# Optimization experiments

Hardware: AMD Instinct MI355X
Metric: run time of the kernel (lower is better)

Reference implementation:

```python
import jax, jax.numpy as jnp
import numpy as np
from jax import lax

B_SZ, SEQ, D_MODEL, D_STATE, DT_RANK = 4, 4096, 256, 16, 16


def setup_inputs() -> dict:
    key = jax.random.key(0)
    ks = jax.random.split(key, 12)
    d, n, r = D_MODEL, D_STATE, DT_RANK
    inp = {}
    inp["hidden_states"] = jax.random.normal(ks[0], (B_SZ, SEQ, d), jnp.float32)
    inp["in_proj_w"] = jax.random.normal(ks[1], (3 * d, d), jnp.float32) * (d ** -0.5)
    inp["x_proj_w"] = jax.random.normal(ks[2], (r + 2 * n, d), jnp.float32) * (d ** -0.5)
    s = r ** -0.5
    inp["dt_proj_w"] = jax.random.uniform(ks[3], (d, r), jnp.float32, -s, s)
    dt = jnp.exp(jax.random.uniform(ks[4], (d,), jnp.float32) * (np.log(0.1) - np.log(1e-3)) + np.log(1e-3))
    inp["dt_proj_b"] = dt + jnp.log(-jnp.expm1(-dt))  # inverse-softplus init
    inp["A_log"] = jnp.log(jnp.broadcast_to(jnp.arange(1, n + 1, dtype=jnp.float32), (d, n)))
    inp["D"] = jnp.ones((d,), jnp.float32)
    inp["out_proj1_w"] = jax.random.normal(ks[5], (d, d), jnp.float32) * (d ** -0.5)
    inp["conv_x_w"] = jax.random.normal(ks[6], (d, 1, 1), jnp.float32)
    inp["conv_x_b"] = jax.random.normal(ks[7], (d,), jnp.float32) * 0.1
    inp["conv_y_w"] = jax.random.normal(ks[8], (d, 1, 3), jnp.float32) * (3 ** -0.5)
    inp["conv_y_b"] = jax.random.normal(ks[9], (d,), jnp.float32) * 0.1
    inp["conv_z_w"] = jax.random.normal(ks[10], (d, 1, 5), jnp.float32) * (5 ** -0.5)
    inp["conv_z_b"] = jax.random.normal(ks[11], (d,), jnp.float32) * 0.1
    return inp


def _silu(x):
    return x * jax.nn.sigmoid(x)


def _dwconv(x, w, b):
    # x: (b, d, l); w: (d, 1, k) depthwise; 'same' padding (odd k)
    k = w.shape[-1]
    pad = (k - 1) // 2
    out = lax.conv_general_dilated(
        x, w, window_strides=(1,), padding=[(pad, pad)],
        dimension_numbers=("NCH", "OIH", "NCH"), feature_group_count=x.shape[1])
    return out + b[None, :, None]


def _selective_scan(u, delta, A, B, C, D, delta_bias):
    # u, delta: (b,d,l); A: (d,n); B,C: (b,n,l); D, delta_bias: (d,)
    delta = jax.nn.softplus(delta + delta_bias[None, :, None])
    dA = jnp.exp(jnp.einsum("bdl,dn->lbdn", delta, A))          # (l,b,d,n)
    dBu = jnp.einsum("bdl,bnl,bdl->lbdn", delta, B, u)           # (l,b,d,n)
    Ct = jnp.transpose(C, (2, 0, 1))                             # (l,b,n)

    def step(h, inp):
        dA_t, dBu_t, C_t = inp
        h = dA_t * h + dBu_t                                     # (b,d,n)
        y = jnp.einsum("bdn,bn->bd", h, C_t)
        return h, y

    h0 = jnp.zeros(u.shape[:2] + (A.shape[1],), u.dtype)
    _, ys = lax.scan(step, h0, (dA, dBu, Ct))                    # ys: (l,b,d)
    y = jnp.transpose(ys, (1, 2, 0))                             # (b,d,l)
    return y + D[None, :, None] * u


def reference(hidden_states, in_proj_w, x_proj_w, dt_proj_w, dt_proj_b, A_log, D,
              out_proj1_w, conv_x_w, conv_x_b, conv_y_w, conv_y_b, conv_z_w, conv_z_b):
    b, l, d = hidden_states.shape
    xyz = jnp.einsum("ble,de->bdl", hidden_states, in_proj_w)    # (b, 3d, l)
    x, y, z = jnp.split(xyz, 3, axis=1)                          # each (b,d,l)
    A = -jnp.exp(A_log.astype(jnp.float32))
    x = _silu(_dwconv(x, conv_x_w, conv_x_b))
    y = _silu(_dwconv(y, conv_y_w, conv_y_b))
    z = _silu(_dwconv(z, conv_z_w, conv_z_b))
    x_dbl = jnp.einsum("bdl,ed->ble", x, x_proj_w)               # (b,l,r+2n)
    dt_r, Bm, Cm = jnp.split(x_dbl, [DT_RANK, DT_RANK + D_STATE], axis=-1)
    # dt_proj applies bias here; selective_scan adds delta_bias again (faithful to source)
    dt = jnp.einsum("blr,dr->bdl", dt_r, dt_proj_w) + dt_proj_b[None, :, None]
    Bm = jnp.transpose(Bm, (0, 2, 1))                            # (b,n,l)
    Cm = jnp.transpose(Cm, (0, 2, 1))
    p = _selective_scan(x, dt, A, Bm, Cm, D.astype(jnp.float32), dt_proj_b.astype(jnp.float32))
    p = jnp.transpose(p, (0, 2, 1))                              # (b,l,d)
    y = jnp.transpose(y, (0, 2, 1))
    z = jnp.transpose(z, (0, 2, 1))
    l1 = jnp.einsum("bld,ed->ble", p * y, out_proj1_w)
    l2 = l1 * z
    l2 = _dwconv(jnp.transpose(l2, (0, 2, 1)), conv_x_w, conv_x_b)
    return jnp.transpose(l2, (0, 2, 1))                          # (b,l,d)
```

## Files before the change

kernel.cpp:

```cpp
#include <hip/hip_runtime.h>
#include <hip/hip_bf16.h>
#include <math.h>

typedef __hip_bfloat16 bf16;
typedef __attribute__((ext_vector_type(8))) short bf16x8;
typedef __attribute__((ext_vector_type(4))) float f32x4;

#define B_SZ 4
#define SEQ  4096
#define DM   256
#define NST  16
#define NCHK 64
#define LC   (SEQ/NCHK)
#define MT   (B_SZ*SEQ)
#define CT   4
#define NLIN (B_SZ*16*256)

__device__ __forceinline__ float silu_f(float v){ return v / (1.f + __expf(-v)); }
__device__ __forceinline__ float softplus_f(float v){
  return (v > 15.f) ? v : __logf(1.f + __expf(v));
}
__device__ __forceinline__ short f2bf(float f){
  union { bf16 h; short s; } u; u.h = __float2bfloat16(f); return u.s;
}
__device__ __forceinline__ float bf2f(short s){
  union { unsigned int i; float f; } v;
  v.i = ((unsigned int)(unsigned short)s) << 16; return v.f;
}
__device__ __forceinline__ float4 bf4_to_f4(uint2 q){
  float4 f;
  f.x = bf2f((short)(q.x & 0xffffu)); f.y = bf2f((short)(q.x >> 16));
  f.z = bf2f((short)(q.y & 0xffffu)); f.w = bf2f((short)(q.y >> 16));
  return f;
}
__device__ __forceinline__ short4 f4_to_bf4(float4 f){
  short4 s; s.x = f2bf(f.x); s.y = f2bf(f.y); s.z = f2bf(f.z); s.w = f2bf(f.w);
  return s;
}

__device__ __forceinline__ void async_cp16(const short* g, short* l){
  __builtin_amdgcn_global_load_lds(
      (const __attribute__((address_space(1))) unsigned int*)g,
      (__attribute__((address_space(3))) unsigned int*)l, 16, 0, 0);
}

template<int CTRL>
__device__ __forceinline__ float dpp_add_step(float v){
  int x = __builtin_amdgcn_update_dpp(0, __float_as_int(v), CTRL, 0xf, 0xf, true);
  return v + __int_as_float(x);
}

__global__ __launch_bounds__(256)
void cvt_in_k(const float* __restrict__ w_in, const float* __restrict__ w_o1,
              const float* __restrict__ hs,
              short* __restrict__ w_in_b, short* __restrict__ w_o1_b,
              short* __restrict__ hsb)
{
  int i = blockIdx.x * 256 + threadIdx.x;
  if (i < 49152) {
    float4 q = *(const float4*)&w_in[i * 4];
    *(short4*)&w_in_b[i * 4] = f4_to_bf4(q);
  } else if (i < 65536) {
    int j = i - 49152;
    float4 q = *(const float4*)&w_o1[j * 4];
    *(short4*)&w_o1_b[j * 4] = f4_to_bf4(q);
  } else {
    int j = i - 65536;
    float4 q = *(const float4*)&hs[(size_t)j * 4];
    *(short4*)&hsb[(size_t)j * 4] = f4_to_bf4(q);
  }
}

template<int EPI, bool OBF>
__global__ __launch_bounds__(256)
void mfma_gemm_k(const short* __restrict__ Av, const short* __restrict__ Bw,
                 void* __restrict__ Outv, int N, int K,
                 const float* __restrict__ bias, const short* __restrict__ zc,
                 const float* __restrict__ cwx)
{
  constexpr int BM = 128, BN = 128, BK = 64;
  __shared__ short As[BM * BK];
  __shared__ short Bs[BN * BK];
  const int tid  = threadIdx.x;
  const int wave = tid >> 6, lane = tid & 63;
  const int quad = lane >> 4, l16 = lane & 15;
  const int wm = (wave & 1) * 64, wn = (wave >> 1) * 64;
  const int m0 = blockIdx.x * BM, n0 = blockIdx.y * BN;

  f32x4 acc[4][4] = {};

  for (int k0 = 0; k0 < K; k0 += BK) {
    #pragma unroll
    for (int p = 0; p < 4; p++) {
      int id = p * 256 + tid;
      int row = id >> 3, slot = id & 7;
      int gch = slot ^ (row & 7);
      async_cp16(Av + (size_t)(m0 + row) * K + k0 + gch * 8,
                 &As[row * 64 + slot * 8]);
      async_cp16(Bw + (size_t)(n0 + row) * K + k0 + gch * 8,
                 &Bs[row * 64 + slot * 8]);
    }
    __syncthreads();
    #pragma unroll
    for (int ks = 0; ks < 2; ks++) {
      bf16x8 fa[4], fb[4];
      #pragma unroll
      for (int i = 0; i < 4; i++) {
        int sa = (ks * 4 + quad) ^ (l16 & 7);
        fa[i] = *(const bf16x8*)&As[(wm + i * 16 + l16) * 64 + sa * 8];
        fb[i] = *(const bf16x8*)&Bs[(wn + i * 16 + l16) * 64 + sa * 8];
      }
      #pragma unroll
      for (int i = 0; i < 4; i++)
        #pragma unroll
        for (int j = 0; j < 4; j++)
          acc[i][j] = __builtin_amdgcn_mfma_f32_16x16x32_bf16(fa[i], fb[j], acc[i][j], 0, 0, 0);
    }
    __syncthreads();
  }

  #pragma unroll
  for (int i = 0; i < 4; i++) {
    #pragma unroll
    for (int j = 0; j < 4; j++) {
      int n = n0 + wn + j * 16 + l16;
      #pragma unroll
      for (int r = 0; r < 4; r++) {
        int m = m0 + wm + i * 16 + quad * 4 + r;
        float v = acc[i][j][r];
        if constexpr (EPI == 2)
          v = v * bf2f(zc[(size_t)m * N + n]) * cwx[n] + bias[n];
        if constexpr (OBF) ((short*)Outv)[(size_t)m * N + n] = f2bf(v);
        else               ((float*)Outv)[(size_t)m * N + n] = v;
      }
    }
  }
}

__global__ __launch_bounds__(256)
void gemm34_k(const short* __restrict__ xcb,
              const float* __restrict__ Bw,
              const float* __restrict__ wdt,
              const float* __restrict__ bdt,
              float* __restrict__ xdbl,
              float* __restrict__ dtv)
{
  constexpr int TM = 32, TK = 16, NN = 48;
  __shared__ __align__(16) float As[TK][TM + 4];
  __shared__ __align__(16) float Bs[TK][64 + 4];
  __shared__ __align__(16) float dt_s[TM][20];
  __shared__ __align__(16) float wdt_s[256][20];
  const int tid = threadIdx.x;
  const int tn = tid & 15, tm = tid >> 4;
  const int m0 = blockIdx.x * TM;
  float acc[2][4] = {};
  const int mlA = tid >> 3, kdA = (tid & 7) * 2;
  const int mlB = tid >> 2, kqB = (tid & 3) * 4;

  {
    float4 q0 = *(const float4*)&wdt[tid * 16 + 0];
    float4 q1 = *(const float4*)&wdt[tid * 16 + 4];
    float4 q2 = *(const float4*)&wdt[tid * 16 + 8];
    float4 q3 = *(const float4*)&wdt[tid * 16 + 12];
    *(float4*)&wdt_s[tid][0]  = q0;
    *(float4*)&wdt_s[tid][4]  = q1;
    *(float4*)&wdt_s[tid][8]  = q2;
    *(float4*)&wdt_s[tid][12] = q3;
  }

  for (int k0 = 0; k0 < 256; k0 += TK) {
    {
      size_t off = (size_t)(m0 + mlA) * 256 + k0 + kdA;
      unsigned int v = *(const unsigned int*)(xcb + off);
      As[kdA + 0][mlA] = bf2f((short)(v & 0xffffu));
      As[kdA + 1][mlA] = bf2f((short)(v >> 16));
    }
    {
      float v0 = 0.f, v1 = 0.f, v2 = 0.f, v3 = 0.f;
      if (mlB < NN) {
        float4 q = *(const float4*)(Bw + (size_t)mlB * 256 + k0 + kqB);
        v0 = q.x; v1 = q.y; v2 = q.z; v3 = q.w;
      }
      Bs[kqB+0][mlB] = v0; Bs[kqB+1][mlB] = v1; Bs[kqB+2][mlB] = v2; Bs[kqB+3][mlB] = v3;
    }
    __syncthreads();
    #pragma unroll
    for (int k = 0; k < TK; k++) {
      float2 av = *(const float2*)&As[k][tm << 1];
      float4 bv = *(const float4*)&Bs[k][tn << 2];
      float a[2] = {av.x, av.y};
      float b[4] = {bv.x, bv.y, bv.z, bv.w};
      #pragma unroll
      for (int i = 0; i < 2; i++)
        #pragma unroll
        for (int j = 0; j < 4; j++)
          acc[i][j] = fmaf(a[i], b[j], acc[i][j]);
    }
    __syncthreads();
  }

  #pragma unroll
  for (int i = 0; i < 2; i++) {
    int m = m0 + (tm << 1) + i;
    #pragma unroll
    for (int j = 0; j < 4; j++) {
      int n = (tn << 2) + j;
      float v = acc[i][j];
      if (n < NN) xdbl[(size_t)m * NN + n] = v;
      if (tn < 4) dt_s[(tm << 1) + i][n] = v;
    }
  }
  __syncthreads();

  const int c0 = tid & 63, rg = tid >> 6;
  float w[4][16];
  float bb[4];
  #pragma unroll
  for (int cc = 0; cc < 4; cc++) {
    int col = cc * 64 + c0;
    #pragma unroll
    for (int q = 0; q < 4; q++) {
      float4 t = *(const float4*)&wdt_s[col][q * 4];
      w[cc][q*4+0] = t.x; w[cc][q*4+1] = t.y; w[cc][q*4+2] = t.z; w[cc][q*4+3] = t.w;
    }
    bb[cc] = 2.f * bdt[col];
  }
  #pragma unroll
  for (int rr = 0; rr < 8; rr++) {
    int row = rg * 8 + rr;
    float dr[16];
    #pragma unroll
    for (int q = 0; q < 4; q++) {
      float4 t = *(const float4*)&dt_s[row][q * 4];
      dr[q*4+0] = t.x; dr[q*4+1] = t.y; dr[q*4+2] = t.z; dr[q*4+3] = t.w;
    }
    #pragma unroll
    for (int cc = 0; cc < 4; cc++) {
      float s = bb[cc];
      #pragma unroll
      for (int k = 0; k < 16; k++) s = fmaf(dr[k], w[cc][k], s);
      dtv[(size_t)(m0 + row) * 256 + cc * 64 + c0] = softplus_f(s);
    }
  }
}

__global__ __launch_bounds__(256)
void conv_silu_k(const short* __restrict__ xyzb,
                 const float* __restrict__ wx, const float* __restrict__ bx,
                 const float* __restrict__ wy, const float* __restrict__ by,
                 const float* __restrict__ wz, const float* __restrict__ bz,
                 short* __restrict__ xcb, short* __restrict__ ycb,
                 short* __restrict__ zcb)
{
  int idx = blockIdx.x * 256 + threadIdx.x;
  int c4 = idx % 192;
  int lt = idx / 192;
  int row0 = lt * CT;
  int l0 = row0 & (SEQ - 1);

  float4 win[CT + 4];
  #pragma unroll
  for (int i = 0; i < CT + 4; i++) {
    int l = l0 + i - 2;
    if (l >= 0 && l < SEQ)
      win[i] = bf4_to_f4(*(const uint2*)(xyzb + (size_t)(row0 + i - 2) * 768 + c4 * 4));
    else
      win[i] = make_float4(0.f, 0.f, 0.f, 0.f);
  }

  if (c4 < 64) {
    int d = c4 * 4;
    float4 w  = *(const float4*)&wx[d];
    float4 bb = *(const float4*)&bx[d];
    #pragma unroll
    for (int t = 0; t < CT; t++) {
      float4 v = win[t + 2], o;
      o.x = silu_f(fmaf(v.x, w.x, bb.x));
      o.y = silu_f(fmaf(v.y, w.y, bb.y));
      o.z = silu_f(fmaf(v.z, w.z, bb.z));
      o.w = silu_f(fmaf(v.w, w.w, bb.w));
      *(short4*)&xcb[(size_t)(row0 + t) * 256 + d] = f4_to_bf4(o);
    }
  } else if (c4 < 128) {
    int d = (c4 - 64) * 4;
    float wq[4][3];
    #pragma unroll
    for (int q = 0; q < 4; q++)
      #pragma unroll
      for (int j = 0; j < 3; j++) wq[q][j] = wy[(d + q) * 3 + j];
    float4 bb = *(const float4*)&by[d];
    #pragma unroll
    for (int t = 0; t < CT; t++) {
      float a0 = bb.x, a1 = bb.y, a2 = bb.z, a3 = bb.w;
      #pragma unroll
      for (int j = 0; j < 3; j++) {
        float4 v = win[t + 1 + j];
        a0 = fmaf(v.x, wq[0][j], a0);
        a1 = fmaf(v.y, wq[1][j], a1);
        a2 = fmaf(v.z, wq[2][j], a2);
        a3 = fmaf(v.w, wq[3][j], a3);
      }
      float4 o; o.x = silu_f(a0); o.y = silu_f(a1); o.z = silu_f(a2); o.w = silu_f(a3);
      *(short4*)&ycb[(size_t)(row0 + t) * 256 + d] = f4_to_bf4(o);
    }
  } else {
    int d = (c4 - 128) * 4;
    float wq[4][5];
    #pragma unroll
    for (int q = 0; q < 4; q++)
      #pragma unroll
      for (int j = 0; j < 5; j++) wq[q][j] = wz[(d + q) * 5 + j];
    float4 bb = *(const float4*)&bz[d];
    #pragma unroll
    for (int t = 0; t < CT; t++) {
      float a0 = bb.x, a1 = bb.y, a2 = bb.z, a3 = bb.w;
      #pragma unroll
      for (int j = 0; j < 5; j++) {
        float4 v = win[t + j];
        a0 = fmaf(v.x, wq[0][j], a0);
        a1 = fmaf(v.y, wq[1][j], a1);
        a2 = fmaf(v.z, wq[2][j], a2);
        a3 = fmaf(v.w, wq[3][j], a3);
      }
      float4 o; o.x = silu_f(a0); o.y = silu_f(a1); o.z = silu_f(a2); o.w = silu_f(a3);
      *(short4*)&zcb[(size_t)(row0 + t) * 256 + d] = f4_to_bf4(o);
    }
  }
}

template<bool PASSC>
__global__ __launch_bounds__(256)
void scan_k(const short* __restrict__ xcb,
            const float* __restrict__ dtv,
            const float* __restrict__ xdbl,
            const float* __restrict__ A_log,
            const float* __restrict__ Dp,
            const float* __restrict__ Hstart,
            float* __restrict__ Pbuf, float* __restrict__ hfbuf,
            const short* __restrict__ ycb,
            short* __restrict__ poutb)
{
  __shared__ __align__(16) float2 du2_s[16 * 66];
  __shared__ __align__(16) float2 BC_s [PASSC ? 16 * 66 : 2];
  __shared__ __align__(16) float  Bc_s [PASSC ? 4 : 16 * 68];
  __shared__ __align__(16) float  y_s  [PASSC ? 16 * 68 : 4];
  const int tid = threadIdx.x;
  const int n = tid & 15, dl = tid >> 4;
  const int ch = blockIdx.x;
  const int d0 = blockIdx.y * 16;
  const int b  = blockIdx.z;
  const int d  = d0 + dl;
  const int t0 = ch * LC;
  const size_t brow = (size_t)b * SEQ;
  const size_t cidx = (size_t)ch * NLIN + ((size_t)b * 16 + blockIdx.y) * 256 + tid;

  float u_r[4];
  #pragma unroll
  for (int i = 0; i < 4; i++) {
    int t = (tid >> 4) + i * 16;
    int dd = tid & 15;
    size_t row = brow + t0 + t;
    float uval = bf2f(xcb[row * 256 + d0 + dd]);
    float dval = dtv[row * 256 + d0 + dd];
    du2_s[dd * 66 + t] = make_float2(dval, dval * uval);
    if constexpr (PASSC) {
      BC_s[dd * 66 + t] = make_float2(xdbl[row * 48 + 16 + dd],
                                      xdbl[row * 48 + 32 + dd]);
      u_r[i] = uval;
    } else {
      Bc_s[dd * 68 + t] = xdbl[row * 48 + 16 + dd];
    }
  }
  __syncthreads();

  const float A_dn = -__expf(A_log[d * NST + n]);

  float h = PASSC ? Hstart[cidx] : 0.f;
  float P = 1.f;
  for (int t4 = 0; t4 < LC; t4 += 4) {
    float4 a = *(const float4*)&du2_s[dl * 66 + t4];
    float4 c = *(const float4*)&du2_s[dl * 66 + t4 + 2];
    float dA[4], du[4];
    dA[0] = __expf(a.x * A_dn); du[0] = a.y;
    dA[1] = __expf(a.z * A_dn); du[1] = a.w;
    dA[2] = __expf(c.x * A_dn); du[2] = c.y;
    dA[3] = __expf(c.z * A_dn); du[3] = c.w;
    if constexpr (!PASSC) {
      float4 f = *(const float4*)&Bc_s[n * 68 + t4];
      float Bv[4] = {f.x, f.y, f.z, f.w};
      #pragma unroll
      for (int j = 0; j < 4; j++) {
        h = fmaf(dA[j], h, du[j] * Bv[j]);
        P *= dA[j];
      }
    } else {
      float4 e = *(const float4*)&BC_s[n * 66 + t4];
      float4 g = *(const float4*)&BC_s[n * 66 + t4 + 2];
      float Bv[4] = {e.x, e.z, g.x, g.z};
      float Cv[4] = {e.y, e.w, g.y, g.w};
      float yv[4];
      #pragma unroll
      for (int j = 0; j < 4; j++) {
        h = fmaf(dA[j], h, du[j] * Bv[j]);
        yv[j] = h * Cv[j];
      }
      #pragma unroll
      for (int j = 0; j < 4; j++) yv[j] = dpp_add_step<0x118>(yv[j]);
      #pragma unroll
      for (int j = 0; j < 4; j++) yv[j] = dpp_add_step<0x114>(yv[j]);
      #pragma unroll
      for (int j = 0; j < 4; j++) yv[j] = dpp_add_step<0x112>(yv[j]);
      #pragma unroll
      for (int j = 0; j < 4; j++) yv[j] = dpp_add_step<0x111>(yv[j]);
      if (n == 15)
        *(float4*)&y_s[dl * 68 + t4] = make_float4(yv[0], yv[1], yv[2], yv[3]);
    }
  }

  if constexpr (!PASSC) {
    Pbuf[cidx] = P;
    hfbuf[cidx] = h;
  } else {
    __syncthreads();
    const float Dval = Dp[d0 + n];
    #pragma unroll
    for (int i = 0; i < 4; i++) {
      int t = (tid >> 4) + i * 16;
      size_t row = brow + t0 + t;
      float p = fmaf(Dval, u_r[i], y_s[n * 68 + t]);
      float yg = bf2f(ycb[row * 256 + d0 + n]);
      poutb[row * 256 + d0 + n] = f2bf(p * yg);
    }
  }
}

__global__ __launch_bounds__(256)
void scan_mid_k(const float* __restrict__ Pbuf, const float* __restrict__ hfbuf,
                float* __restrict__ Hstart)
{
  int lin = blockIdx.x * 256 + threadIdx.x;
  float H = 0.f;
  for (int c = 0; c < NCHK; c++) {
    size_t idx = (size_t)c * NLIN + lin;
    Hstart[idx] = H;
    H = Pbuf[idx] * H + hfbuf[idx];
  }
}

extern "C" void kernel_launch(void* const* d_in, const int* in_sizes, int n_in,
                              void* d_out, int out_size, void* d_ws, size_t ws_size,
                              hipStream_t stream)
{
  const float* hs    = (const float*)d_in[0];
  const float* w_in  = (const float*)d_in[1];
  const float* w_xp  = (const float*)d_in[2];
  const float* w_dt  = (const float*)d_in[3];
  const float* b_dt  = (const float*)d_in[4];
  const float* A_log = (const float*)d_in[5];
  const float* Dp    = (const float*)d_in[6];
  const float* w_o1  = (const float*)d_in[7];
  const float* cwx   = (const float*)d_in[8];
  const float* cbx   = (const float*)d_in[9];
  const float* cwy   = (const float*)d_in[10];
  const float* cby   = (const float*)d_in[11];
  const float* cwz   = (const float*)d_in[12];
  const float* cbz   = (const float*)d_in[13];

  char* wsb = (char*)d_ws;
  short* xyzb = (short*)wsb;
  short* xcb  = (short*)(wsb + (size_t)MT * 768 * 2);
  short* ycb  = xcb + (size_t)MT * 256;
  short* zcb  = ycb + (size_t)MT * 256;
  short* pbufb= zcb + (size_t)MT * 256;
  short* w_in_b = pbufb + (size_t)MT * 256;
  short* w_o1_b = w_in_b + 768 * 256;
  short* hsb  = w_o1_b + 256 * 256;
  float* xdbl = (float*)(hsb + (size_t)MT * 256 + 128);
  float* dtv  = xdbl + (size_t)MT * 48;
  float* Pb   = dtv  + (size_t)MT * 256;
  float* hf   = Pb   + (size_t)NCHK * NLIN;
  float* Hs   = hf   + (size_t)NCHK * NLIN;

  dim3 blk(256);

  cvt_in_k<<<dim3(4352), blk, 0, stream>>>(w_in, w_o1, hs, w_in_b, w_o1_b, hsb);

  mfma_gemm_k<0, true><<<dim3(MT / 128, 768 / 128), blk, 0, stream>>>(
      hsb, w_in_b, xyzb, 768, 256, nullptr, nullptr, nullptr);

  conv_silu_k<<<dim3((MT / CT) * 192 / 256), blk, 0, stream>>>(
      xyzb, cwx, cbx, cwy, cby, cwz, cbz, xcb, ycb, zcb);

  gemm34_k<<<dim3(MT / 32), blk, 0, stream>>>(
      xcb, w_xp, w_dt, b_dt, xdbl, dtv);

  scan_k<false><<<dim3(NCHK, DM / 16, B_SZ), blk, 0, stream>>>(
      xcb, dtv, xdbl, A_log, Dp, nullptr, Pb, hf, nullptr, nullptr);
  scan_mid_k<<<dim3(NLIN / 256), blk, 0, stream>>>(Pb, hf, Hs);
  scan_k<true><<<dim3(NCHK, DM / 16, B_SZ), blk, 0, stream>>>(
      xcb, dtv, xdbl, A_log, Dp, Hs, nullptr, nullptr, ycb, pbufb);

  mfma_gemm_k<2, false><<<dim3(MT / 128, 256 / 128), blk, 0, stream>>>(
      pbufb, w_o1_b, d_out, 256, 256, cbx, zcb, cwx);
}
```

Measured before the change: 201.5 us.

## Fuse input bf16 conversion into GEMM, shrink GEMM tile, store delta as bf16

The separate fp32-to-bf16 conversion of hidden_states is removed. The input-projection GEMM now loads fp32 activations and converts them to bf16 while staging into shared memory. The GEMM block tile changes from 128x128 to 64x128, which doubles the number of blocks and lowers per-wave accumulator use. The softplus delta tensor is written and read as bf16 instead of fp32, halving its traffic into the two scan passes at the cost of lower precision in delta.

```diff
diff --git a/kernel.cpp b/kernel.cpp
--- a/kernel.cpp
+++ b/kernel.cpp
@@ -51,69 +51,85 @@
 }
 
 __global__ __launch_bounds__(256)
-void cvt_in_k(const float* __restrict__ w_in, const float* __restrict__ w_o1,
-              const float* __restrict__ hs,
-              short* __restrict__ w_in_b, short* __restrict__ w_o1_b,
-              short* __restrict__ hsb)
+void cvt_w_k(const float* __restrict__ w_in, const float* __restrict__ w_o1,
+             short* __restrict__ w_in_b, short* __restrict__ w_o1_b)
 {
   int i = blockIdx.x * 256 + threadIdx.x;
   if (i < 49152) {
     float4 q = *(const float4*)&w_in[i * 4];
     *(short4*)&w_in_b[i * 4] = f4_to_bf4(q);
-  } else if (i < 65536) {
+  } else {
     int j = i - 49152;
     float4 q = *(const float4*)&w_o1[j * 4];
     *(short4*)&w_o1_b[j * 4] = f4_to_bf4(q);
-  } else {
-    int j = i - 65536;
-    float4 q = *(const float4*)&hs[(size_t)j * 4];
-    *(short4*)&hsb[(size_t)j * 4] = f4_to_bf4(q);
-  }
-}
-
-template<int EPI, bool OBF>
+  }
+}
+
+template<int EPI, bool OBF, bool AFP32>
 __global__ __launch_bounds__(256)
-void mfma_gemm_k(const short* __restrict__ Av, const short* __restrict__ Bw,
+void mfma_gemm_k(const void* __restrict__ Av, const short* __restrict__ Bw,
                  void* __restrict__ Outv, int N, int K,
                  const float* __restrict__ bias, const short* __restrict__ zc,
                  const float* __restrict__ cwx)
 {
-  constexpr int BM = 128, BN = 128, BK = 64;
-  __shared__ short As[BM * BK];
+  constexpr int BM = 64, BN = 128, BK = 64;
+  constexpr int LDA = AFP32 ? 72 : 64;
+  __shared__ short As[BM * LDA];
   __shared__ short Bs[BN * BK];
   const int tid  = threadIdx.x;
   const int wave = tid >> 6, lane = tid & 63;
   const int quad = lane >> 4, l16 = lane & 15;
-  const int wm = (wave & 1) * 64, wn = (wave >> 1) * 64;
+  const int wn = wave * 32;
   const int m0 = blockIdx.x * BM, n0 = blockIdx.y * BN;
 
-  f32x4 acc[4][4] = {};
+  f32x4 acc[4][2] = {};
 
   for (int k0 = 0; k0 < K; k0 += BK) {
+    if constexpr (AFP32) {
+      int row = tid >> 2, kq = (tid & 3) * 16;
+      const float* ga = (const float*)Av + (size_t)(m0 + row) * K + k0 + kq;
+      #pragma unroll
+      for (int q = 0; q < 4; q++) {
+        float4 v = *(const float4*)(ga + q * 4);
+        *(short4*)&As[row * LDA + kq + q * 4] = f4_to_bf4(v);
+      }
+    } else {
+      #pragma unroll
+      for (int p = 0; p < 2; p++) {
+        int id = p * 256 + tid;
+        int row = id >> 3, slot = id & 7;
+        int gch = slot ^ (row & 7);
+        async_cp16((const short*)Av + (size_t)(m0 + row) * K + k0 + gch * 8,
+                   &As[row * 64 + slot * 8]);
+      }
+    }
     #pragma unroll
     for (int p = 0; p < 4; p++) {
       int id = p * 256 + tid;
       int row = id >> 3, slot = id & 7;
       int gch = slot ^ (row & 7);
-      async_cp16(Av + (size_t)(m0 + row) * K + k0 + gch * 8,
-                 &As[row * 64 + slot * 8]);
       async_cp16(Bw + (size_t)(n0 + row) * K + k0 + gch * 8,
                  &Bs[row * 64 + slot * 8]);
     }
     __syncthreads();
     #pragma unroll
     for (int ks = 0; ks < 2; ks++) {
-      bf16x8 fa[4], fb[4];
+      bf16x8 fa[4], fb[2];
+      int sb = (ks * 4 + quad) ^ (l16 & 7);
       #pragma unroll
       for (int i = 0; i < 4; i++) {
-        int sa = (ks * 4 + quad) ^ (l16 & 7);
-        fa[i] = *(const bf16x8*)&As[(wm + i * 16 + l16) * 64 + sa * 8];
-        fb[i] = *(const bf16x8*)&Bs[(wn + i * 16 + l16) * 64 + sa * 8];
-      }
+        if constexpr (AFP32)
+          fa[i] = *(const bf16x8*)&As[(i * 16 + l16) * LDA + (ks * 4 + quad) * 8];
+        else
+          fa[i] = *(const bf16x8*)&As[(i * 16 + l16) * 64 + sb * 8];
+      }
+      #pragma unroll
+      for (int j = 0; j < 2; j++)
+        fb[j] = *(const bf16x8*)&Bs[(wn + j * 16 + l16) * 64 + sb * 8];
       #pragma unroll
       for (int i = 0; i < 4; i++)
         #pragma unroll
-        for (int j = 0; j < 4; j++)
+        for (int j = 0; j < 2; j++)
           acc[i][j] = __builtin_amdgcn_mfma_f32_16x16x32_bf16(fa[i], fb[j], acc[i][j], 0, 0, 0);
     }
     __syncthreads();
@@ -122,11 +138,11 @@
   #pragma unroll
   for (int i = 0; i < 4; i++) {
     #pragma unroll
-    for (int j = 0; j < 4; j++) {
+    for (int j = 0; j < 2; j++) {
       int n = n0 + wn + j * 16 + l16;
       #pragma unroll
       for (int r = 0; r < 4; r++) {
-        int m = m0 + wm + i * 16 + quad * 4 + r;
+        int m = m0 + i * 16 + quad * 4 + r;
         float v = acc[i][j][r];
         if constexpr (EPI == 2)
           v = v * bf2f(zc[(size_t)m * N + n]) * cwx[n] + bias[n];
@@ -143,7 +159,7 @@
               const float* __restrict__ wdt,
               const float* __restrict__ bdt,
               float* __restrict__ xdbl,
-              float* __restrict__ dtv)
+              short* __restrict__ dtvb)
 {
   constexpr int TM = 32, TK = 16, NN = 48;
   __shared__ __align__(16) float As[TK][TM + 4];
@@ -239,7 +255,7 @@
       float s = bb[cc];
       #pragma unroll
       for (int k = 0; k < 16; k++) s = fmaf(dr[k], w[cc][k], s);
-      dtv[(size_t)(m0 + row) * 256 + cc * 64 + c0] = softplus_f(s);
+      dtvb[(size_t)(m0 + row) * 256 + cc * 64 + c0] = f2bf(softplus_f(s));
     }
   }
 }
@@ -331,7 +347,7 @@
 template<bool PASSC>
 __global__ __launch_bounds__(256)
 void scan_k(const short* __restrict__ xcb,
-            const float* __restrict__ dtv,
+            const short* __restrict__ dtvb,
             const float* __restrict__ xdbl,
             const float* __restrict__ A_log,
             const float* __restrict__ Dp,
@@ -361,7 +377,7 @@
     int dd = tid & 15;
     size_t row = brow + t0 + t;
     float uval = bf2f(xcb[row * 256 + d0 + dd]);
-    float dval = dtv[row * 256 + d0 + dd];
+    float dval = bf2f(dtvb[row * 256 + d0 + dd]);
     du2_s[dd * 66 + t] = make_float2(dval, dval * uval);
     if constexpr (PASSC) {
       BC_s[dd * 66 + t] = make_float2(xdbl[row * 48 + 16 + dd],
@@ -474,32 +490,31 @@
   short* pbufb= zcb + (size_t)MT * 256;
   short* w_in_b = pbufb + (size_t)MT * 256;
   short* w_o1_b = w_in_b + 768 * 256;
-  short* hsb  = w_o1_b + 256 * 256;
-  float* xdbl = (float*)(hsb + (size_t)MT * 256 + 128);
-  float* dtv  = xdbl + (size_t)MT * 48;
-  float* Pb   = dtv  + (size_t)MT * 256;
+  short* dtvb = w_o1_b + 256 * 256;
+  float* xdbl = (float*)(dtvb + (size_t)MT * 256 + 128);
+  float* Pb   = xdbl + (size_t)MT * 48;
   float* hf   = Pb   + (size_t)NCHK * NLIN;
   float* Hs   = hf   + (size_t)NCHK * NLIN;
 
   dim3 blk(256);
 
-  cvt_in_k<<<dim3(4352), blk, 0, stream>>>(w_in, w_o1, hs, w_in_b, w_o1_b, hsb);
-
-  mfma_gemm_k<0, true><<<dim3(MT / 128, 768 / 128), blk, 0, stream>>>(
-      hsb, w_in_b, xyzb, 768, 256, nullptr, nullptr, nullptr);
+  cvt_w_k<<<dim3(256), blk, 0, stream>>>(w_in, w_o1, w_in_b, w_o1_b);
+
+  mfma_gemm_k<0, true, true><<<dim3(MT / 64, 768 / 128), blk, 0, stream>>>(
+      hs, w_in_b, xyzb, 768, 256, nullptr, nullptr, nullptr);
 
   conv_silu_k<<<dim3((MT / CT) * 192 / 256), blk, 0, stream>>>(
       xyzb, cwx, cbx, cwy, cby, cwz, cbz, xcb, ycb, zcb);
 
   gemm34_k<<<dim3(MT / 32), blk, 0, stream>>>(
-      xcb, w_xp, w_dt, b_dt, xdbl, dtv);
+      xcb, w_xp, w_dt, b_dt, xdbl, dtvb);
 
   scan_k<false><<<dim3(NCHK, DM / 16, B_SZ), blk, 0, stream>>>(
-      xcb, dtv, xdbl, A_log, Dp, nullptr, Pb, hf, nullptr, nullptr);
+      xcb, dtvb, xdbl, A_log, Dp, nullptr, Pb, hf, nullptr, nullptr);
   scan_mid_k<<<dim3(NLIN / 256), blk, 0, stream>>>(Pb, hf, Hs);
   scan_k<true><<<dim3(NCHK, DM / 16, B_SZ), blk, 0, stream>>>(
-      xcb, dtv, xdbl, A_log, Dp, Hs, nullptr, nullptr, ycb, pbufb);
-
-  mfma_gemm_k<2, false><<<dim3(MT / 128, 256 / 128), blk, 0, stream>>>(
+      xcb, dtvb, xdbl, A_log, Dp, Hs, nullptr, nullptr, ycb, pbufb);
+
+  mfma_gemm_k<2, false, false><<<dim3(MT / 64, 256 / 128), blk, 0, stream>>>(
       pbufb, w_o1_b, d_out, 256, 256, cbx, zcb, cwx);
 }
```

New measurement: 201.5 us. No clear change (+0.0%).
